# Performance work log

Measured on AMD Instinct MI355X. Metric: run time of the kernel, lower is better.

Reference implementation:

```python
import jax, jax.numpy as jnp
import numpy as np

B, T, C = 4, 2048, 768
H, N = 12, 64
N_LAYER, LAYER_ID = 12, 1
EPS_GN = 0.00064


def setup_inputs():
    key = jax.random.key(0)
    ks = jax.random.split(key, 20)
    r01 = LAYER_ID / (N_LAYER - 1)
    r10 = 1.0 - LAYER_ID / N_LAYER
    ddd = (np.arange(C, dtype=np.float64) / C)[None, None, :]

    def lam(p, off=0.0):
        return jnp.asarray(1.0 - np.power(ddd, p) - off, dtype=jnp.float32)

    decay = -7.0 + 5.0 * (np.arange(C, dtype=np.float64) / (C - 1)) ** (0.85 + r01 ** 0.5)

    def rn(i, shape, scale):
        return scale * jax.random.normal(ks[i], shape, jnp.float32)

    s = 1.0 / C ** 0.5
    return {
        "x": jax.random.normal(ks[0], (B, T, C), jnp.float32),
        "v_first": jax.random.normal(ks[1], (B, T, C), jnp.float32),
        "lambda_r": lam(0.2 * r10), "lambda_w": lam(0.9 * r10),
        "lambda_k": lam(0.9 * r10, 0.4 * r01), "lambda_v": lam(0.4 * r10, 0.6 * r01),
        "lambda_a": lam(0.9 * r10), "lambda_g": lam(0.2 * r10),
        "w_miu": jnp.asarray(decay[None, None, :] + 0.5, jnp.float32),
        "w_A": rn(2, (C, 64), 0.02), "w_B": rn(3, (64, C), 0.02),
        "a_miu": jnp.zeros((1, 1, C), jnp.float32),
        "a_A": rn(4, (C, 64), 0.02), "a_B": rn(5, (64, C), 0.02),
        "v_miu": jnp.ones((1, 1, C), jnp.float32),
        "v_A": rn(6, (C, 64), 0.02), "v_B": rn(7, (64, C), 0.02),
        "g_A": rn(8, (C, 128), 0.02), "g_B": rn(9, (128, C), 0.02),
        "k_k": 0.85 * jnp.ones((1, 1, C), jnp.float32),
        "k_a": jnp.ones((1, 1, C), jnp.float32),
        "r_k": rn(10, (H, N), 0.02),
        "W_r": jax.random.uniform(ks[11], (C, C), jnp.float32, -0.5 * s, 0.5 * s),
        "W_k": jax.random.uniform(ks[12], (C, C), jnp.float32, -0.05 * s, 0.05 * s),
        "W_v": jax.random.uniform(ks[13], (C, C), jnp.float32, -0.5 * s, 0.5 * s),
        "W_o": rn(14, (C, C), 0.02),
        "ln_w": jnp.ones((C,), jnp.float32), "ln_b": jnp.zeros((C,), jnp.float32),
    }


def _wkv7(r, w, k, v, z, b):
    # r,w,k,v,z,b: (B,T,H,N). RWKV-7 linear recurrence with per-head NxN state:
    # S_t = S_{t-1}*diag(exp(-exp(w_t))) + (S_{t-1} z_t) b_t^T + v_t k_t^T ; y_t = S_t r_t
    decay = jnp.exp(-jnp.exp(w))

    def step(S, inp):
        rt, dt, kt, vt, zt, bt = inp  # each (B,H,N)
        sa = jnp.einsum('bhij,bhj->bhi', S, zt)
        S = S * dt[:, :, None, :] + sa[..., None] * bt[:, :, None, :] + vt[..., None] * kt[:, :, None, :]
        y = jnp.einsum('bhij,bhj->bhi', S, rt)
        return S, y

    seq = tuple(jnp.moveaxis(t, 1, 0) for t in (r, decay, k, v, z, b))  # (T,B,H,N)
    S0 = jnp.zeros((r.shape[0], r.shape[2], r.shape[3], r.shape[3]), r.dtype)
    _, ys = jax.lax.scan(step, S0, seq)
    return jnp.moveaxis(ys, 0, 1)  # (B,T,H,N)


def reference(x, v_first, lambda_r, lambda_w, lambda_k, lambda_v, lambda_a, lambda_g,
              w_miu, w_A, w_B, a_miu, a_A, a_B, v_miu, v_A, v_B, g_A, g_B,
              k_k, k_a, r_k, W_r, W_k, W_v, W_o, ln_w, ln_b):
    Bb, Tt, Cc = x.shape
    # ZeroPad2d((0,0,1,-1)): shift sequence right by 1, zero at t=0
    x_shift = jnp.pad(x, ((0, 0), (1, 0), (0, 0)))[:, :-1]
    xd = x_shift - x
    r = (x + xd * lambda_r) @ W_r.T
    w = x + xd * lambda_w
    k = (x + xd * lambda_k) @ W_k.T
    v = (x + xd * lambda_v) @ W_v.T
    a_in = x + xd * lambda_a
    g_in = x + xd * lambda_g
    if LAYER_ID == 0:
        v_first = v
    else:
        v = v + (v_first - v) * jax.nn.sigmoid(v_miu + (v @ v_A) @ v_B)
    w = -jax.nn.softplus(-(w_miu + jnp.tanh(w @ w_A) @ w_B)) - 0.5
    a = jax.nn.sigmoid(a_miu + (a_in @ a_A) @ a_B)
    g = jax.nn.sigmoid(g_in @ g_A) @ g_B
    kk = (k * k_k).reshape(Bb, Tt, H, N)
    kk = kk / jnp.maximum(jnp.linalg.norm(kk, axis=-1, keepdims=True), 1e-12)
    k = k * (1 + (a - 1) * k_a)
    rh = r.reshape(Bb, Tt, H, N)
    wh = w.reshape(Bb, Tt, H, N)
    kh = k.reshape(Bb, Tt, H, N)
    vh = v.reshape(Bb, Tt, H, N)
    ah = a.reshape(Bb, Tt, H, N)
    y = _wkv7(rh, wh, kh, vh, -kk, kk * ah)  # (B,T,H,N)
    # GroupNorm over heads, eps=0.00064, biased variance (torch semantics)
    mu = y.mean(-1, keepdims=True)
    var = y.var(-1, keepdims=True)
    y = ((y - mu) / jnp.sqrt(var + EPS_GN)).reshape(Bb, Tt, Cc) * ln_w + ln_b
    y = y + ((rh * kh * r_k).sum(-1, keepdims=True) * vh).reshape(Bb, Tt, Cc)
    out = (y * g) @ W_o.T
    return (out, v_first)
```

## Files before the change

kernel.cpp:

```cpp
#include <hip/hip_runtime.h>
#include <hip/hip_bf16.h>
#include <math.h>


#define B_  4
#define T_  2048
#define C_  768
#define H_  12

typedef __attribute__((ext_vector_type(8))) short bf16x8;
typedef __attribute__((ext_vector_type(4))) float f32x4;

#define GLD16(gsrc, ldst)                                                     \
  __builtin_amdgcn_global_load_lds(                                           \
      (const __attribute__((address_space(1))) void*)(gsrc),                  \
      (__attribute__((address_space(3))) void*)(ldst), 16, 0, 0)

template <int CTRL>
static __device__ __forceinline__ float row_ror_add(float v) {
  int t = __builtin_amdgcn_update_dpp(0, __float_as_int(v), CTRL, 0xF, 0xF, true);
  return v + __int_as_float(t);
}
static __device__ __forceinline__ float row_sum16(float v) {
  v = row_ror_add<0x128>(v);
  v = row_ror_add<0x124>(v);
  v = row_ror_add<0x122>(v);
  v = row_ror_add<0x121>(v);
  return v;
}

static __device__ __forceinline__ float wave_sum64(float v) {
  v = row_sum16(v);
  v += __shfl_xor(v, 16);
  v += __shfl_xor(v, 32);
  return v;
}

static __device__ __forceinline__ short bf16b(float f) {
  __hip_bfloat16 h = __float2bfloat16(f);
  return *reinterpret_cast<short*>(&h);
}

enum { EPI_NONE = 0, EPI_TANH, EPI_WDECAY, EPI_SIGBIAS, EPI_SIGMOID, EPI_VMIX };

static __device__ __forceinline__ float apply_epi_f(int EPI, float val, int n,
                                                    int gmrow, int N,
                                                    const float* bias,
                                                    const float* ex1,
                                                    const float* ex2) {
  if (EPI == EPI_TANH) {
    val = tanhf(val);
  } else if (EPI == EPI_WDECAY) {
    const float u = bias[n] + val;
    const float sig = 1.f / (1.f + expf(-u));
    val = expf(-0.60653065971263342f * sig);
  } else if (EPI == EPI_SIGBIAS) {
    const float u = bias[n] + val;
    val = 1.f / (1.f + expf(-u));
  } else if (EPI == EPI_SIGMOID) {
    val = 1.f / (1.f + expf(-val));
  } else if (EPI == EPI_VMIX) {
    const float u = bias[n] + val;
    const float sg = 1.f / (1.f + expf(-u));
    const size_t off = (size_t)gmrow * N + n;
    const float v0v = ex1[off];
    const float vf = ex2[off];
    val = v0v + (vf - v0v) * sg;
  }
  return val;
}

template <int EPI, bool DUAL>
__global__ __launch_bounds__(256) void gemm_epi_k(
    const short* __restrict__ A, const short* __restrict__ Bw,
    float* __restrict__ C, short* __restrict__ C16, int M, int N, int K,
    const float* __restrict__ bias, const float* __restrict__ ex1,
    const float* __restrict__ ex2) {
  __shared__ short As[128 * 32];
  __shared__ short Bs[128 * 32];
  const int tid = threadIdx.x;
  const int wave = tid >> 6, lane = tid & 63;
  const int m0 = blockIdx.y * 128, n0 = blockIdx.x * 128;
  const int wm = (wave >> 1) * 64, wn = (wave & 1) * 64;
  const int fr = lane & 15, fk = (lane >> 4) * 8;

  f32x4 acc[4][4];
#pragma unroll
  for (int i = 0; i < 4; i++)
#pragma unroll
    for (int j = 0; j < 4; j++) acc[i][j] = (f32x4){0.f, 0.f, 0.f, 0.f};

  const int srow = tid >> 2, scol = (tid & 3) * 8;
  const short* gA = A + (size_t)(m0 + srow) * K + scol;
  const short* gB = Bw + (size_t)(n0 + srow) * K + scol;
  short* lA0 = &As[wave * 512];
  short* lA1 = &As[2048 + wave * 512];
  short* lB0 = &Bs[wave * 512];
  short* lB1 = &Bs[2048 + wave * 512];

  for (int k0 = 0; k0 < K; k0 += 32) {
    GLD16(gA + k0, lA0);
    GLD16(gA + (size_t)64 * K + k0, lA1);
    GLD16(gB + k0, lB0);
    GLD16(gB + (size_t)64 * K + k0, lB1);
    __syncthreads();

    bf16x8 af[4], bf[4];
#pragma unroll
    for (int i = 0; i < 4; i++)
      af[i] = *(const bf16x8*)&As[(wm + i * 16 + fr) * 32 + fk];
#pragma unroll
    for (int j = 0; j < 4; j++)
      bf[j] = *(const bf16x8*)&Bs[(wn + j * 16 + fr) * 32 + fk];
#pragma unroll
    for (int i = 0; i < 4; i++)
#pragma unroll
      for (int j = 0; j < 4; j++)
        acc[i][j] =
            __builtin_amdgcn_mfma_f32_16x16x32_bf16(af[i], bf[j], acc[i][j], 0, 0, 0);
    __syncthreads();
  }

#pragma unroll
  for (int i = 0; i < 4; i++) {
    const int gm = m0 + wm + i * 16 + (lane >> 4) * 4;
#pragma unroll
    for (int j = 0; j < 4; j++) {
      const int gn = n0 + wn + j * 16 + fr;
#pragma unroll
      for (int rix = 0; rix < 4; rix++) {
        float val = acc[i][j][rix];
        val = apply_epi_f(EPI, val, gn, gm + rix, N, bias, ex1, ex2);
        C[(size_t)(gm + rix) * N + gn] = val;
        if (DUAL) C16[(size_t)(gm + rix) * N + gn] = bf16b(val);
      }
    }
  }
}

template <int EPI>
__global__ __launch_bounds__(256) void gemm_s1_k(
    const short* __restrict__ A, const short* __restrict__ Bw,
    short* __restrict__ out16, int M, int N, int K) {
  __shared__ short As[128 * 32];
  __shared__ short Bs[64 * 32];
  const int tid = threadIdx.x;
  const int wave = tid >> 6, lane = tid & 63;
  const int m0 = blockIdx.y * 128, n0 = blockIdx.x * 64;
  const int wm = (wave >> 1) * 64, wn = (wave & 1) * 32;
  const int fr = lane & 15, fk = (lane >> 4) * 8;

  f32x4 acc[4][2];
#pragma unroll
  for (int i = 0; i < 4; i++)
#pragma unroll
    for (int j = 0; j < 2; j++) acc[i][j] = (f32x4){0.f, 0.f, 0.f, 0.f};

  const int srow = tid >> 2, scol = (tid & 3) * 8;
  const short* gA = A + (size_t)(m0 + srow) * K + scol;
  const short* gB = Bw + (size_t)(n0 + srow) * K + scol;
  short* lA0 = &As[wave * 512];
  short* lA1 = &As[2048 + wave * 512];
  short* lB0 = &Bs[wave * 512];

  for (int k0 = 0; k0 < K; k0 += 32) {
    GLD16(gA + k0, lA0);
    GLD16(gA + (size_t)64 * K + k0, lA1);
    GLD16(gB + k0, lB0);
    __syncthreads();

    bf16x8 af[4], bf[2];
#pragma unroll
    for (int i = 0; i < 4; i++)
      af[i] = *(const bf16x8*)&As[(wm + i * 16 + fr) * 32 + fk];
#pragma unroll
    for (int j = 0; j < 2; j++)
      bf[j] = *(const bf16x8*)&Bs[(wn + j * 16 + fr) * 32 + fk];
#pragma unroll
    for (int i = 0; i < 4; i++)
#pragma unroll
      for (int j = 0; j < 2; j++)
        acc[i][j] =
            __builtin_amdgcn_mfma_f32_16x16x32_bf16(af[i], bf[j], acc[i][j], 0, 0, 0);
    __syncthreads();
  }

#pragma unroll
  for (int i = 0; i < 4; i++) {
    const int gm = m0 + wm + i * 16 + (lane >> 4) * 4;
#pragma unroll
    for (int j = 0; j < 2; j++) {
      const int gn = n0 + wn + j * 16 + fr;
#pragma unroll
      for (int rix = 0; rix < 4; rix++) {
        float val = acc[i][j][rix];
        if (EPI == EPI_TANH) val = tanhf(val);
        else if (EPI == EPI_SIGMOID) val = 1.f / (1.f + expf(-val));
        out16[(size_t)(gm + rix) * N + gn] = bf16b(val);
      }
    }
  }
}

__global__ __launch_bounds__(256) void mix6_k(
    const float* __restrict__ x, const float* __restrict__ lr,
    const float* __restrict__ lk, const float* __restrict__ lv,
    const float* __restrict__ lw, const float* __restrict__ la,
    const float* __restrict__ lg, short* __restrict__ xr,
    short* __restrict__ xk, short* __restrict__ xv, short* __restrict__ xw,
    short* __restrict__ xa, short* __restrict__ xg) {
  const int i = blockIdx.x * 256 + threadIdx.x;
  const int c4 = i % (C_ / 4);
  const int gm = i / (C_ / 4);
  const float4 xa4 = ((const float4*)x)[i];
  float4 xp = make_float4(0.f, 0.f, 0.f, 0.f);
  if ((gm % T_) != 0) xp = ((const float4*)x)[i - C_ / 4];
  const float4 dx =
      make_float4(xp.x - xa4.x, xp.y - xa4.y, xp.z - xa4.z, xp.w - xa4.w);

#define MIXOUT(dst, lam)                                                      \
  {                                                                           \
    const float4 l4 = ((const float4*)lam)[c4];                               \
    short4 o = {bf16b(fmaf(dx.x, l4.x, xa4.x)),                               \
                bf16b(fmaf(dx.y, l4.y, xa4.y)),                               \
                bf16b(fmaf(dx.z, l4.z, xa4.z)),                               \
                bf16b(fmaf(dx.w, l4.w, xa4.w))};                              \
    ((short4*)dst)[i] = o;                                                    \
  }
  MIXOUT(xr, lr);
  MIXOUT(xk, lk);
  MIXOUT(xv, lv);
  MIXOUT(xw, lw);
  MIXOUT(xa, la);
  MIXOUT(xg, lg);
#undef MIXOUT
}

__global__ __launch_bounds__(256) void cvtw4_k(
    const float* __restrict__ w0, const float* __restrict__ w1,
    const float* __restrict__ w2, const float* __restrict__ w3,
    short* __restrict__ o0, short* __restrict__ o1s,
    short* __restrict__ o2s, short* __restrict__ o3s, int n4) {
  const int i = blockIdx.x * 256 + threadIdx.x;
  if (i >= n4) return;
  const float* src;
  short* dst;
  switch (blockIdx.y) {
    case 0: src = w0; dst = o0; break;
    case 1: src = w1; dst = o1s; break;
    case 2: src = w2; dst = o2s; break;
    default: src = w3; dst = o3s; break;
  }
  const float4 v = ((const float4*)src)[i];
  short4 o = {bf16b(v.x), bf16b(v.y), bf16b(v.z), bf16b(v.w)};
  ((short4*)dst)[i] = o;
}

__global__ __launch_bounds__(256) void cvtT8_k(
    const float* __restrict__ i0, const float* __restrict__ i1,
    const float* __restrict__ i2, const float* __restrict__ i3,
    const float* __restrict__ i4, const float* __restrict__ i5,
    const float* __restrict__ i6, const float* __restrict__ i7,
    short* __restrict__ o0, short* __restrict__ o1,
    short* __restrict__ o2, short* __restrict__ o3,
    short* __restrict__ o4, short* __restrict__ o5,
    short* __restrict__ o6, short* __restrict__ o7) {
  const float* in;
  short* out;
  int R, Cc;
  switch (blockIdx.y) {
    case 0: in = i0; out = o0; R = C_; Cc = 64; break;
    case 1: in = i1; out = o1; R = C_; Cc = 64; break;
    case 2: in = i2; out = o2; R = C_; Cc = 64; break;
    case 3: in = i3; out = o3; R = C_; Cc = 128; break;
    case 4: in = i4; out = o4; R = 64; Cc = C_; break;
    case 5: in = i5; out = o5; R = 64; Cc = C_; break;
    case 6: in = i6; out = o6; R = 64; Cc = C_; break;
    default: in = i7; out = o7; R = 128; Cc = C_; break;
  }
  const int n = R * Cc;
  for (int i = blockIdx.x * 256 + threadIdx.x; i < n; i += gridDim.x * 256) {
    const int r = i / Cc, c = i % Cc;
    out[(size_t)c * R + r] = bf16b(in[i]);
  }
}

__global__ __launch_bounds__(256) void kkprep_k(
    const float* __restrict__ k0, const float* __restrict__ a,
    const float* __restrict__ k_k, const float* __restrict__ k_a,
    float* __restrict__ kout, float* __restrict__ z, float* __restrict__ bb) {
  const int wid = threadIdx.x >> 6;
  const int lane = threadIdx.x & 63;
  const size_t hid = (size_t)blockIdx.x * 4 + wid;
  const int h = (int)(hid % H_);
  const size_t idx = hid * 64 + lane;
  const int c = h * 64 + lane;
  const float kv = k0[idx];
  const float av = a[idx];
  const float kk = kv * k_k[c];
  const float ss = wave_sum64(kk * kk);
  const float denom = fmaxf(sqrtf(ss), 1e-12f);
  const float kkn = kk / denom;
  z[idx] = -kkn;
  bb[idx] = kkn * av;
  kout[idx] = kv * (1.f + (av - 1.f) * k_a[c]);
}

#define CH 16
#define NC (T_ / CH)
__global__ __launch_bounds__(256) void wkv7_k(
    const float* __restrict__ rr, const float* __restrict__ dd,
    const float* __restrict__ kk, const float* __restrict__ vv,
    const float* __restrict__ zz, const float* __restrict__ bbv,
    float* __restrict__ yy) {
  __shared__ float lds[2][6 * CH * 64];
  const int blk = blockIdx.x;
  const int bh = blk % 48;
  const int rq = blk / 48;
  const int b = bh / H_, h = bh % H_;
  const int tid = threadIdx.x;
  const int wave = tid >> 6;
  const int l = tid & 63;
  const int l16 = l & 15;
  const int row = rq * 16 + wave * 4 + (l >> 4);
  const int cb = l16 * 4;
  const size_t btb = (size_t)b * T_;

  const size_t g0 = (btb + wave * 4 + (l >> 4)) * C_ + h * 64 + cb;
  const int dbase = wave * 256;

#define STAGE(BUF, GOFF)                                                      \
  {                                                                           \
    float* Ld = &lds[BUF][0];                                                 \
    GLD16(dd + (GOFF), Ld + 0 * 1024 + dbase);                                \
    GLD16(zz + (GOFF), Ld + 1 * 1024 + dbase);                                \
    GLD16(bbv + (GOFF), Ld + 2 * 1024 + dbase);                               \
    GLD16(kk + (GOFF), Ld + 3 * 1024 + dbase);                                \
    GLD16(rr + (GOFF), Ld + 4 * 1024 + dbase);                                \
    GLD16(vv + (GOFF), Ld + 5 * 1024 + dbase);                                \
  }

#define LDSTEP(S_, TL_)                                                       \
  {                                                                           \
    Wf[S_] = *(const float4*)&Lb[0 * 1024 + (TL_) * 64 + cb];                 \
    Zf[S_] = *(const float4*)&Lb[1 * 1024 + (TL_) * 64 + cb];                 \
    Bf[S_] = *(const float4*)&Lb[2 * 1024 + (TL_) * 64 + cb];                 \
    Kf[S_] = *(const float4*)&Lb[3 * 1024 + (TL_) * 64 + cb];                 \
    Rf[S_] = *(const float4*)&Lb[4 * 1024 + (TL_) * 64 + cb];                 \
    Vf[S_] = Lb[5 * 1024 + (TL_) * 64 + row];                                 \
  }

  STAGE(0, g0);
  __syncthreads();

  float S0 = 0.f, S1 = 0.f, S2 = 0.f, S3 = 0.f;
  size_t gpf = g0 + (size_t)CH * C_;
  const size_t ybase = btb * C_ + h * 64 + row;

  for (int c = 0; c < NC; ++c) {
    if (c + 1 < NC) STAGE((c + 1) & 1, gpf);
    gpf += (size_t)CH * C_;
    const float* Lb = lds[c & 1];

    float4 Wf[3], Zf[3], Bf[3], Kf[3], Rf[3];
    float Vf[3];
    LDSTEP(0, 0);
    LDSTEP(1, 1);
#pragma unroll
    for (int tl = 0; tl < CH; ++tl) {
      const int sl = tl % 3;
      if (tl + 2 < CH) {
        const int s2 = (tl + 2) % 3;
        LDSTEP(s2, tl + 2);
      }
      const float4 w4 = Wf[sl], z4 = Zf[sl], b4 = Bf[sl], k4 = Kf[sl],
                   r4 = Rf[sl];
      const float vi = Vf[sl];

      float sa = fmaf(S1, z4.y, S0 * z4.x) + fmaf(S3, z4.w, S2 * z4.z);
      sa = row_sum16(sa);

      S0 = fmaf(S0, w4.x, fmaf(sa, b4.x, vi * k4.x));
      S1 = fmaf(S1, w4.y, fmaf(sa, b4.y, vi * k4.y));
      S2 = fmaf(S2, w4.z, fmaf(sa, b4.z, vi * k4.z));
      S3 = fmaf(S3, w4.w, fmaf(sa, b4.w, vi * k4.w));

      float yp = fmaf(S1, r4.y, S0 * r4.x) + fmaf(S3, r4.w, S2 * r4.z);
      yp = row_sum16(yp);
      if (l16 == 0) yy[ybase + (size_t)(c * CH + tl) * C_] = yp;
    }
    __syncthreads();
  }
#undef STAGE
#undef LDSTEP
}

__global__ __launch_bounds__(256) void gn_k(
    const float* __restrict__ y, const float* __restrict__ r,
    const float* __restrict__ k, const float* __restrict__ v,
    const float* __restrict__ g, const float* __restrict__ r_k,
    const float* __restrict__ ln_w, const float* __restrict__ ln_b,
    short* __restrict__ ymb) {
  const int wid = threadIdx.x >> 6;
  const int lane = threadIdx.x & 63;
  const size_t hid = (size_t)blockIdx.x * 4 + wid;
  const int h = (int)(hid % H_);
  const size_t idx = hid * 64 + lane;
  const int c = h * 64 + lane;

  const float yv = y[idx];
  const float mu = wave_sum64(yv) * (1.f / 64.f);
  const float sq = wave_sum64(yv * yv) * (1.f / 64.f);
  const float var = sq - mu * mu;
  float yn = (yv - mu) * rsqrtf(var + 0.00064f);
  yn = yn * ln_w[c] + ln_b[c];

  const float s = wave_sum64(r[idx] * k[idx] * r_k[c]);
  yn += s * v[idx];
  ymb[idx] = bf16b(yn * g[idx]);
}

__global__ __launch_bounds__(256) void copy4_k(const float4* __restrict__ src,
                                               float4* __restrict__ dst, int n4) {
  const int i = blockIdx.x * blockDim.x + threadIdx.x;
  if (i < n4) dst[i] = src[i];
}

extern "C" void kernel_launch(void* const* d_in, const int* in_sizes, int n_in,
                              void* d_out, int out_size, void* d_ws,
                              size_t ws_size, hipStream_t stream) {
  const float* x       = (const float*)d_in[0];
  const float* v_first = (const float*)d_in[1];
  const float* lam_r   = (const float*)d_in[2];
  const float* lam_w   = (const float*)d_in[3];
  const float* lam_k   = (const float*)d_in[4];
  const float* lam_v   = (const float*)d_in[5];
  const float* lam_a   = (const float*)d_in[6];
  const float* lam_g   = (const float*)d_in[7];
  const float* w_miu   = (const float*)d_in[8];
  const float* w_A     = (const float*)d_in[9];
  const float* w_B     = (const float*)d_in[10];
  const float* a_miu   = (const float*)d_in[11];
  const float* a_A     = (const float*)d_in[12];
  const float* a_B     = (const float*)d_in[13];
  const float* v_miu   = (const float*)d_in[14];
  const float* v_A     = (const float*)d_in[15];
  const float* v_B     = (const float*)d_in[16];
  const float* g_A     = (const float*)d_in[17];
  const float* g_B     = (const float*)d_in[18];
  const float* k_k     = (const float*)d_in[19];
  const float* k_a     = (const float*)d_in[20];
  const float* r_k     = (const float*)d_in[21];
  const float* W_r     = (const float*)d_in[22];
  const float* W_k     = (const float*)d_in[23];
  const float* W_v     = (const float*)d_in[24];
  const float* W_o     = (const float*)d_in[25];
  const float* ln_w    = (const float*)d_in[26];
  const float* ln_b    = (const float*)d_in[27];

  const int M = B_ * T_;
  const size_t S = (size_t)M * C_;

  float* ws   = (float*)d_ws;
  float* r_   = ws + 0 * S;
  float* kbuf = ws + 1 * S;
  float* vbuf = ws + 2 * S;
  float* dec_ = ws + 3 * S;
  float* a_   = ws + 4 * S;
  float* g_   = ws + 5 * S;
  float* z_   = ws + 6 * S;
  float* bb_  = ws + 7 * S;
  float* h_   = ws + 8 * S;
  short* wb   = (short*)(h_ + (size_t)M * 128);
  float* out  = (float*)d_out;

  const int WN = C_ * C_;
  short* wrb = wb + 0 * (size_t)WN;
  short* wkb = wb + 1 * (size_t)WN;
  short* wvb = wb + 2 * (size_t)WN;
  short* wob = wb + 3 * (size_t)WN;
  short* wAT = wb + 4 * (size_t)WN;
  short* aAT = wAT + (size_t)C_ * 64;
  short* vAT = aAT + (size_t)C_ * 64;
  short* gAT = vAT + (size_t)C_ * 64;
  short* wBT = gAT + (size_t)C_ * 128;
  short* aBT = wBT + (size_t)C_ * 64;
  short* vBT = aBT + (size_t)C_ * 64;
  short* gBT = vBT + (size_t)C_ * 64;

  short* xr  = (short*)dec_;
  short* xk  = (short*)a_;
  short* xv  = (short*)g_;
  short* xw  = (short*)z_;
  short* xa  = (short*)z_ + S;
  short* xg  = (short*)bb_;
  short* vbuf16 = (short*)bb_ + S;
  short* h_w = (short*)h_;
  short* h_a = h_w + (size_t)M * 64;
  short* h_g = h_a + (size_t)M * 64;
  short* h_v = (short*)dec_ + S;
  short* ymb = (short*)z_;

  {
    dim3 blk(256), grid(WN / 4 / 256, 4);
    hipLaunchKernelGGL(cvtw4_k, grid, blk, 0, stream, W_r, W_k, W_v, W_o,
                       wrb, wkb, wvb, wob, WN / 4);
  }
  {
    dim3 blk(256), grid((C_ * 128 + 255) / 256, 8);
    hipLaunchKernelGGL(cvtT8_k, grid, blk, 0, stream, w_A, a_A, v_A, g_A,
                       w_B, a_B, v_B, g_B, wAT, aAT, vAT, gAT, wBT, aBT, vBT,
                       gBT);
  }
  {
    dim3 blk(256), grid((int)(S / 4 / 256));
    hipLaunchKernelGGL(mix6_k, grid, blk, 0, stream, x, lam_r, lam_k, lam_v,
                       lam_w, lam_a, lam_g, xr, xk, xv, xw, xa, xg);
  }
  {
    dim3 blk(256), grid(C_ / 128, M / 128);
    hipLaunchKernelGGL((gemm_epi_k<EPI_NONE, false>), grid, blk, 0, stream,
                       xr, wrb, r_, (short*)nullptr, M, C_, C_, nullptr,
                       nullptr, nullptr);
    hipLaunchKernelGGL((gemm_epi_k<EPI_NONE, false>), grid, blk, 0, stream,
                       xk, wkb, kbuf, (short*)nullptr, M, C_, C_, nullptr,
                       nullptr, nullptr);
    hipLaunchKernelGGL((gemm_epi_k<EPI_NONE, true>), grid, blk, 0, stream,
                       xv, wvb, vbuf, vbuf16, M, C_, C_, nullptr, nullptr,
                       nullptr);
  }
  {
    dim3 blk(256);
    dim3 g64(1, M / 128), g128(2, M / 128);
    hipLaunchKernelGGL((gemm_s1_k<EPI_TANH>), g64, blk, 0, stream, xw, wAT,
                       h_w, M, 64, C_);
    hipLaunchKernelGGL((gemm_s1_k<EPI_NONE>), g64, blk, 0, stream, xa, aAT,
                       h_a, M, 64, C_);
    hipLaunchKernelGGL((gemm_s1_k<EPI_SIGMOID>), g128, blk, 0, stream, xg,
                       gAT, h_g, M, 128, C_);
    hipLaunchKernelGGL((gemm_s1_k<EPI_NONE>), g64, blk, 0, stream, vbuf16,
                       vAT, h_v, M, 64, C_);
  }
  {
    dim3 blk(256), grid(C_ / 128, M / 128);
    hipLaunchKernelGGL((gemm_epi_k<EPI_VMIX, false>), grid, blk, 0, stream,
                       h_v, vBT, vbuf, (short*)nullptr, M, C_, 64, v_miu,
                       vbuf, v_first);
    hipLaunchKernelGGL((gemm_epi_k<EPI_WDECAY, false>), grid, blk, 0, stream,
                       h_w, wBT, dec_, (short*)nullptr, M, C_, 64, w_miu,
                       nullptr, nullptr);
    hipLaunchKernelGGL((gemm_epi_k<EPI_SIGBIAS, false>), grid, blk, 0, stream,
                       h_a, aBT, a_, (short*)nullptr, M, C_, 64, a_miu,
                       nullptr, nullptr);
    hipLaunchKernelGGL((gemm_epi_k<EPI_NONE, false>), grid, blk, 0, stream,
                       h_g, gBT, g_, (short*)nullptr, M, C_, 128, nullptr,
                       nullptr, nullptr);
  }
  {
    dim3 grid((B_ * T_ * H_) / 4), blk(256);
    hipLaunchKernelGGL(kkprep_k, grid, blk, 0, stream, kbuf, a_, k_k, k_a,
                       kbuf, z_, bb_);
  }
  {
    dim3 grid(B_ * H_ * 4), blk(256);
    hipLaunchKernelGGL(wkv7_k, grid, blk, 0, stream, r_, dec_, kbuf, vbuf, z_,
                       bb_, a_);
  }
  {
    dim3 grid((B_ * T_ * H_) / 4), blk(256);
    hipLaunchKernelGGL(gn_k, grid, blk, 0, stream, a_, r_, kbuf, vbuf, g_, r_k,
                       ln_w, ln_b, ymb);
  }
  {
    dim3 blk(256), grid(C_ / 128, M / 128);
    hipLaunchKernelGGL((gemm_epi_k<EPI_NONE, false>), grid, blk, 0, stream,
                       ymb, wob, out, (short*)nullptr, M, C_, C_, nullptr,
                       nullptr, nullptr);
  }
  {
    const int n4 = (int)(S / 4);
    dim3 grid((n4 + 255) / 256), blk(256);
    hipLaunchKernelGGL(copy4_k, grid, blk, 0, stream, (const float4*)v_first,
                       (float4*)(out + S), n4);
  }
}
```

Baseline: 754.3 us.

## Batch GEMM launches into multi-role kernels and overlap g-projection with WKV scan

Replaces the many separate GEMM launches with grouped kernels that pick their matrices by block index: r/k/v in one launch, the four low-rank first stages in one, and three second stages in one. The g second-stage GEMM and the v_first copy now run as extra blocks inside the WKV recurrence launch, using GPUs left idle by the 192 scan blocks. The scan reads v straight from global memory into registers, prefetched one chunk ahead, instead of staging it through LDS, and the weight conversions are merged into a single launch. This cuts launch count and idle time, but epilogue selection is now a runtime branch rather than a template parameter, and the 48 g-GEMM blocks loop serially over 8 tiles each, so they may finish after the scan blocks.

Result: faster. 738.4 us (-2.1%).

```diff
diff --git a/kernel.cpp b/kernel.cpp
--- a/kernel.cpp
+++ b/kernel.cpp
@@ -43,23 +43,23 @@
 
 enum { EPI_NONE = 0, EPI_TANH, EPI_WDECAY, EPI_SIGBIAS, EPI_SIGMOID, EPI_VMIX };
 
-static __device__ __forceinline__ float apply_epi_f(int EPI, float val, int n,
+static __device__ __forceinline__ float apply_epi_f(int epi, float val, int n,
                                                     int gmrow, int N,
                                                     const float* bias,
                                                     const float* ex1,
                                                     const float* ex2) {
-  if (EPI == EPI_TANH) {
+  if (epi == EPI_TANH) {
     val = tanhf(val);
-  } else if (EPI == EPI_WDECAY) {
+  } else if (epi == EPI_WDECAY) {
     const float u = bias[n] + val;
     const float sig = 1.f / (1.f + expf(-u));
     val = expf(-0.60653065971263342f * sig);
-  } else if (EPI == EPI_SIGBIAS) {
+  } else if (epi == EPI_SIGBIAS) {
     const float u = bias[n] + val;
     val = 1.f / (1.f + expf(-u));
-  } else if (EPI == EPI_SIGMOID) {
+  } else if (epi == EPI_SIGMOID) {
     val = 1.f / (1.f + expf(-val));
-  } else if (EPI == EPI_VMIX) {
+  } else if (epi == EPI_VMIX) {
     const float u = bias[n] + val;
     const float sg = 1.f / (1.f + expf(-u));
     const size_t off = (size_t)gmrow * N + n;
@@ -70,17 +70,14 @@
   return val;
 }
 
-template <int EPI, bool DUAL>
-__global__ __launch_bounds__(256) void gemm_epi_k(
+static __device__ __forceinline__ void gemm128_tile(
     const short* __restrict__ A, const short* __restrict__ Bw,
     float* __restrict__ C, short* __restrict__ C16, int M, int N, int K,
-    const float* __restrict__ bias, const float* __restrict__ ex1,
-    const float* __restrict__ ex2) {
-  __shared__ short As[128 * 32];
-  __shared__ short Bs[128 * 32];
+    int bx, int by, int epi, const float* bias, const float* ex1,
+    const float* ex2, short* As, short* Bs) {
   const int tid = threadIdx.x;
   const int wave = tid >> 6, lane = tid & 63;
-  const int m0 = blockIdx.y * 128, n0 = blockIdx.x * 128;
+  const int m0 = by * 128, n0 = bx * 128;
   const int wm = (wave >> 1) * 64, wn = (wave & 1) * 64;
   const int fr = lane & 15, fk = (lane >> 4) * 8;
 
@@ -130,23 +127,21 @@
 #pragma unroll
       for (int rix = 0; rix < 4; rix++) {
         float val = acc[i][j][rix];
-        val = apply_epi_f(EPI, val, gn, gm + rix, N, bias, ex1, ex2);
+        val = apply_epi_f(epi, val, gn, gm + rix, N, bias, ex1, ex2);
         C[(size_t)(gm + rix) * N + gn] = val;
-        if (DUAL) C16[(size_t)(gm + rix) * N + gn] = bf16b(val);
+        if (C16) C16[(size_t)(gm + rix) * N + gn] = bf16b(val);
       }
     }
   }
 }
 
-template <int EPI>
-__global__ __launch_bounds__(256) void gemm_s1_k(
+static __device__ __forceinline__ void gemm64_tile(
     const short* __restrict__ A, const short* __restrict__ Bw,
-    short* __restrict__ out16, int M, int N, int K) {
-  __shared__ short As[128 * 32];
-  __shared__ short Bs[64 * 32];
+    short* __restrict__ out16, int M, int N, int K, int bx, int by, int epi,
+    short* As, short* Bs) {
   const int tid = threadIdx.x;
   const int wave = tid >> 6, lane = tid & 63;
-  const int m0 = blockIdx.y * 128, n0 = blockIdx.x * 64;
+  const int m0 = by * 128, n0 = bx * 64;
   const int wm = (wave >> 1) * 64, wn = (wave & 1) * 32;
   const int fr = lane & 15, fk = (lane >> 4) * 8;
 
@@ -194,12 +189,85 @@
 #pragma unroll
       for (int rix = 0; rix < 4; rix++) {
         float val = acc[i][j][rix];
-        if (EPI == EPI_TANH) val = tanhf(val);
-        else if (EPI == EPI_SIGMOID) val = 1.f / (1.f + expf(-val));
+        if (epi == EPI_TANH) val = tanhf(val);
+        else if (epi == EPI_SIGMOID) val = 1.f / (1.f + expf(-val));
         out16[(size_t)(gm + rix) * N + gn] = bf16b(val);
       }
     }
   }
+}
+
+__global__ __launch_bounds__(256) void big3_k(
+    const short* __restrict__ xr, const short* __restrict__ xk,
+    const short* __restrict__ xv, const short* __restrict__ wrb,
+    const short* __restrict__ wkb, const short* __restrict__ wvb,
+    float* __restrict__ r_, float* __restrict__ kbuf,
+    float* __restrict__ vbuf, short* __restrict__ vbuf16) {
+  __shared__ short smem[2 * 128 * 32];
+  const int role = blockIdx.x / 6, bx = blockIdx.x % 6;
+  const short* A;
+  const short* Bw;
+  float* C;
+  short* C16 = nullptr;
+  if (role == 0) { A = xr; Bw = wrb; C = r_; }
+  else if (role == 1) { A = xk; Bw = wkb; C = kbuf; }
+  else { A = xv; Bw = wvb; C = vbuf; C16 = vbuf16; }
+  gemm128_tile(A, Bw, C, C16, B_ * T_, C_, C_, bx, blockIdx.y, EPI_NONE,
+               nullptr, nullptr, nullptr, smem, smem + 128 * 32);
+}
+
+__global__ __launch_bounds__(256) void s1x4_k(
+    const short* __restrict__ xw, const short* __restrict__ xa,
+    const short* __restrict__ xg, const short* __restrict__ vbuf16,
+    const short* __restrict__ wAT, const short* __restrict__ aAT,
+    const short* __restrict__ gAT, const short* __restrict__ vAT,
+    short* __restrict__ h_w, short* __restrict__ h_a,
+    short* __restrict__ h_g, short* __restrict__ h_v) {
+  __shared__ short smem[128 * 32 + 64 * 32];
+  const int bx = blockIdx.x;
+  const short* A;
+  const short* Bw;
+  short* O;
+  int N, tb, epi;
+  if (bx == 0)      { A = xw;     Bw = wAT; O = h_w; N = 64;  tb = 0; epi = EPI_TANH; }
+  else if (bx == 1) { A = xa;     Bw = aAT; O = h_a; N = 64;  tb = 0; epi = EPI_NONE; }
+  else if (bx == 2) { A = xg;     Bw = gAT; O = h_g; N = 128; tb = 0; epi = EPI_SIGMOID; }
+  else if (bx == 3) { A = xg;     Bw = gAT; O = h_g; N = 128; tb = 1; epi = EPI_SIGMOID; }
+  else              { A = vbuf16; Bw = vAT; O = h_v; N = 64;  tb = 0; epi = EPI_NONE; }
+  gemm64_tile(A, Bw, O, B_ * T_, N, C_, tb, blockIdx.y, epi, smem,
+              smem + 128 * 32);
+}
+
+__global__ __launch_bounds__(256) void s2x3_k(
+    const short* __restrict__ h_v, const short* __restrict__ h_w,
+    const short* __restrict__ h_a, const short* __restrict__ vBT,
+    const short* __restrict__ wBT, const short* __restrict__ aBT,
+    float* __restrict__ vbuf, float* __restrict__ dec_, float* __restrict__ a_,
+    const float* __restrict__ v_miu, const float* __restrict__ w_miu,
+    const float* __restrict__ a_miu, const float* __restrict__ v_first) {
+  __shared__ short smem[2 * 128 * 32];
+  const int role = blockIdx.x / 6, bx = blockIdx.x % 6;
+  const short* A;
+  const short* Bw;
+  float* C;
+  const float* bias;
+  const float* ex1 = nullptr;
+  const float* ex2 = nullptr;
+  int epi;
+  if (role == 0) { A = h_v; Bw = vBT; C = vbuf; bias = v_miu; ex1 = vbuf; ex2 = v_first; epi = EPI_VMIX; }
+  else if (role == 1) { A = h_w; Bw = wBT; C = dec_; bias = w_miu; epi = EPI_WDECAY; }
+  else { A = h_a; Bw = aBT; C = a_; bias = a_miu; epi = EPI_SIGBIAS; }
+  gemm128_tile(A, Bw, C, nullptr, B_ * T_, C_, 64, bx, blockIdx.y, epi, bias,
+               ex1, ex2, smem, smem + 128 * 32);
+}
+
+__global__ __launch_bounds__(256) void outp_k(
+    const short* __restrict__ ymb, const short* __restrict__ wob,
+    float* __restrict__ out) {
+  __shared__ short smem[2 * 128 * 32];
+  gemm128_tile(ymb, wob, out, nullptr, B_ * T_, C_, C_, blockIdx.x,
+               blockIdx.y, EPI_NONE, nullptr, nullptr, nullptr, smem,
+               smem + 128 * 32);
 }
 
 __global__ __launch_bounds__(256) void mix6_k(
@@ -236,52 +304,49 @@
 #undef MIXOUT
 }
 
-__global__ __launch_bounds__(256) void cvtw4_k(
-    const float* __restrict__ w0, const float* __restrict__ w1,
-    const float* __restrict__ w2, const float* __restrict__ w3,
-    short* __restrict__ o0, short* __restrict__ o1s,
-    short* __restrict__ o2s, short* __restrict__ o3s, int n4) {
-  const int i = blockIdx.x * 256 + threadIdx.x;
-  if (i >= n4) return;
-  const float* src;
-  short* dst;
-  switch (blockIdx.y) {
-    case 0: src = w0; dst = o0; break;
-    case 1: src = w1; dst = o1s; break;
-    case 2: src = w2; dst = o2s; break;
-    default: src = w3; dst = o3s; break;
-  }
-  const float4 v = ((const float4*)src)[i];
-  short4 o = {bf16b(v.x), bf16b(v.y), bf16b(v.z), bf16b(v.w)};
-  ((short4*)dst)[i] = o;
-}
-
-__global__ __launch_bounds__(256) void cvtT8_k(
-    const float* __restrict__ i0, const float* __restrict__ i1,
-    const float* __restrict__ i2, const float* __restrict__ i3,
-    const float* __restrict__ i4, const float* __restrict__ i5,
-    const float* __restrict__ i6, const float* __restrict__ i7,
-    short* __restrict__ o0, short* __restrict__ o1,
-    short* __restrict__ o2, short* __restrict__ o3,
-    short* __restrict__ o4, short* __restrict__ o5,
-    short* __restrict__ o6, short* __restrict__ o7) {
-  const float* in;
-  short* out;
-  int R, Cc;
-  switch (blockIdx.y) {
-    case 0: in = i0; out = o0; R = C_; Cc = 64; break;
-    case 1: in = i1; out = o1; R = C_; Cc = 64; break;
-    case 2: in = i2; out = o2; R = C_; Cc = 64; break;
-    case 3: in = i3; out = o3; R = C_; Cc = 128; break;
-    case 4: in = i4; out = o4; R = 64; Cc = C_; break;
-    case 5: in = i5; out = o5; R = 64; Cc = C_; break;
-    case 6: in = i6; out = o6; R = 64; Cc = C_; break;
-    default: in = i7; out = o7; R = 128; Cc = C_; break;
-  }
-  const int n = R * Cc;
-  for (int i = blockIdx.x * 256 + threadIdx.x; i < n; i += gridDim.x * 256) {
-    const int r = i / Cc, c = i % Cc;
-    out[(size_t)c * R + r] = bf16b(in[i]);
+__global__ __launch_bounds__(256) void wprep_k(
+    const float* __restrict__ W_r, const float* __restrict__ W_k,
+    const float* __restrict__ W_v, const float* __restrict__ W_o,
+    const float* __restrict__ w_A, const float* __restrict__ a_A,
+    const float* __restrict__ v_A, const float* __restrict__ g_A,
+    const float* __restrict__ w_B, const float* __restrict__ a_B,
+    const float* __restrict__ v_B, const float* __restrict__ g_B,
+    short* __restrict__ wrb, short* __restrict__ wkb,
+    short* __restrict__ wvb, short* __restrict__ wob,
+    short* __restrict__ wAT, short* __restrict__ aAT,
+    short* __restrict__ vAT, short* __restrict__ gAT,
+    short* __restrict__ wBT, short* __restrict__ aBT,
+    short* __restrict__ vBT, short* __restrict__ gBT) {
+  const int job = blockIdx.y;
+  const int WN = C_ * C_;
+  if (job < 4) {
+    const float* src = (job == 0) ? W_r : (job == 1) ? W_k : (job == 2) ? W_v : W_o;
+    short* dst = (job == 0) ? wrb : (job == 1) ? wkb : (job == 2) ? wvb : wob;
+    const int n4 = WN / 4;
+    for (int i = blockIdx.x * 256 + threadIdx.x; i < n4; i += gridDim.x * 256) {
+      const float4 v = ((const float4*)src)[i];
+      short4 o = {bf16b(v.x), bf16b(v.y), bf16b(v.z), bf16b(v.w)};
+      ((short4*)dst)[i] = o;
+    }
+  } else {
+    const float* in;
+    short* out;
+    int R, Cc;
+    switch (job) {
+      case 4: in = w_A; out = wAT; R = C_; Cc = 64; break;
+      case 5: in = a_A; out = aAT; R = C_; Cc = 64; break;
+      case 6: in = v_A; out = vAT; R = C_; Cc = 64; break;
+      case 7: in = g_A; out = gAT; R = C_; Cc = 128; break;
+      case 8: in = w_B; out = wBT; R = 64; Cc = C_; break;
+      case 9: in = a_B; out = aBT; R = 64; Cc = C_; break;
+      case 10: in = v_B; out = vBT; R = 64; Cc = C_; break;
+      default: in = g_B; out = gBT; R = 128; Cc = C_; break;
+    }
+    const int n = R * Cc;
+    for (int i = blockIdx.x * 256 + threadIdx.x; i < n; i += gridDim.x * 256) {
+      const int r = i / Cc, c = i % Cc;
+      out[(size_t)c * R + r] = bf16b(in[i]);
+    }
   }
 }
 
@@ -308,13 +373,35 @@
 
 #define CH 16
 #define NC (T_ / CH)
-__global__ __launch_bounds__(256) void wkv7_k(
+__global__ __launch_bounds__(256) void wkv7f_k(
     const float* __restrict__ rr, const float* __restrict__ dd,
     const float* __restrict__ kk, const float* __restrict__ vv,
     const float* __restrict__ zz, const float* __restrict__ bbv,
-    float* __restrict__ yy) {
-  __shared__ float lds[2][6 * CH * 64];
+    float* __restrict__ yy, const short* __restrict__ h_g,
+    const short* __restrict__ gBT, float* __restrict__ g_,
+    const float4* __restrict__ cpsrc, float4* __restrict__ cpdst, int n4) {
+  __shared__ __align__(16) char smem[2 * 5 * CH * 64 * 4];
   const int blk = blockIdx.x;
+
+  if (blk >= 240) {
+    const int rb = blk - 240;
+    for (int i = rb * 256 + threadIdx.x; i < n4; i += 16 * 256)
+      cpdst[i] = cpsrc[i];
+    return;
+  }
+  if (blk >= 192) {
+    short* As = (short*)smem;
+    short* Bs = As + 128 * 32;
+    const int rb = blk - 192;
+    for (int it = 0; it < 8; ++it) {
+      const int tile = rb + it * 48;
+      gemm128_tile(h_g, gBT, g_, nullptr, B_ * T_, C_, 128, tile % 6,
+                   tile / 6, EPI_NONE, nullptr, nullptr, nullptr, As, Bs);
+    }
+    return;
+  }
+
+  float* lds = (float*)smem;
   const int bh = blk % 48;
   const int rq = blk / 48;
   const int b = bh / H_, h = bh % H_;
@@ -328,16 +415,16 @@
 
   const size_t g0 = (btb + wave * 4 + (l >> 4)) * C_ + h * 64 + cb;
   const int dbase = wave * 256;
+  const size_t vrow0 = btb * C_ + h * 64 + row;
 
 #define STAGE(BUF, GOFF)                                                      \
   {                                                                           \
-    float* Ld = &lds[BUF][0];                                                 \
+    float* Ld = lds + (BUF) * 5120;                                           \
     GLD16(dd + (GOFF), Ld + 0 * 1024 + dbase);                                \
     GLD16(zz + (GOFF), Ld + 1 * 1024 + dbase);                                \
     GLD16(bbv + (GOFF), Ld + 2 * 1024 + dbase);                               \
     GLD16(kk + (GOFF), Ld + 3 * 1024 + dbase);                                \
     GLD16(rr + (GOFF), Ld + 4 * 1024 + dbase);                                \
-    GLD16(vv + (GOFF), Ld + 5 * 1024 + dbase);                                \
   }
 
 #define LDSTEP(S_, TL_)                                                       \
@@ -347,52 +434,72 @@
     Bf[S_] = *(const float4*)&Lb[2 * 1024 + (TL_) * 64 + cb];                 \
     Kf[S_] = *(const float4*)&Lb[3 * 1024 + (TL_) * 64 + cb];                 \
     Rf[S_] = *(const float4*)&Lb[4 * 1024 + (TL_) * 64 + cb];                 \
-    Vf[S_] = Lb[5 * 1024 + (TL_) * 64 + row];                                 \
-  }
-
+  }
+
+#define PREFV(ARR, CC)                                                        \
+  {                                                                           \
+    const size_t vb = vrow0 + (size_t)(CC) * CH * C_;                         \
+    _Pragma("unroll") for (int j = 0; j < CH; ++j)                            \
+        ARR[j] = vv[vb + (size_t)j * C_];                                     \
+  }
+
+#define CHUNK_BODY(VARR, CIDX)                                                \
+  {                                                                           \
+    float4 Wf[3], Zf[3], Bf[3], Kf[3], Rf[3];                                 \
+    LDSTEP(0, 0);                                                             \
+    LDSTEP(1, 1);                                                             \
+    _Pragma("unroll") for (int tl = 0; tl < CH; ++tl) {                       \
+      const int sl = tl % 3;                                                  \
+      if (tl + 2 < CH) { LDSTEP((tl + 2) % 3, tl + 2); }                      \
+      const float4 w4 = Wf[sl], z4 = Zf[sl], b4 = Bf[sl], k4 = Kf[sl],        \
+                   r4 = Rf[sl];                                               \
+      const float vi = VARR[tl];                                              \
+      float sa = fmaf(S1, z4.y, S0 * z4.x) + fmaf(S3, z4.w, S2 * z4.z);       \
+      sa = row_sum16(sa);                                                     \
+      S0 = fmaf(S0, w4.x, fmaf(sa, b4.x, vi * k4.x));                         \
+      S1 = fmaf(S1, w4.y, fmaf(sa, b4.y, vi * k4.y));                         \
+      S2 = fmaf(S2, w4.z, fmaf(sa, b4.z, vi * k4.z));                         \
+      S3 = fmaf(S3, w4.w, fmaf(sa, b4.w, vi * k4.w));                         \
+      float yp = fmaf(S1, r4.y, S0 * r4.x) + fmaf(S3, r4.w, S2 * r4.z);       \
+      yp = row_sum16(yp);                                                     \
+      if (l16 == 0) yy[ybase + (size_t)((CIDX)*CH + tl) * C_] = yp;           \
+    }                                                                         \
+  }
+
+  float vA[CH], vB[CH];
   STAGE(0, g0);
+  PREFV(vA, 0);
   __syncthreads();
 
   float S0 = 0.f, S1 = 0.f, S2 = 0.f, S3 = 0.f;
   size_t gpf = g0 + (size_t)CH * C_;
   const size_t ybase = btb * C_ + h * 64 + row;
 
-  for (int c = 0; c < NC; ++c) {
-    if (c + 1 < NC) STAGE((c + 1) & 1, gpf);
+  for (int c = 0; c < NC; c += 2) {
+    PREFV(vB, c + 1);
+    STAGE(1, gpf);
     gpf += (size_t)CH * C_;
-    const float* Lb = lds[c & 1];
-
-    float4 Wf[3], Zf[3], Bf[3], Kf[3], Rf[3];
-    float Vf[3];
-    LDSTEP(0, 0);
-    LDSTEP(1, 1);
-#pragma unroll
-    for (int tl = 0; tl < CH; ++tl) {
-      const int sl = tl % 3;
-      if (tl + 2 < CH) {
-        const int s2 = (tl + 2) % 3;
-        LDSTEP(s2, tl + 2);
-      }
-      const float4 w4 = Wf[sl], z4 = Zf[sl], b4 = Bf[sl], k4 = Kf[sl],
-                   r4 = Rf[sl];
-      const float vi = Vf[sl];
-
-      float sa = fmaf(S1, z4.y, S0 * z4.x) + fmaf(S3, z4.w, S2 * z4.z);
-      sa = row_sum16(sa);
-
-      S0 = fmaf(S0, w4.x, fmaf(sa, b4.x, vi * k4.x));
-      S1 = fmaf(S1, w4.y, fmaf(sa, b4.y, vi * k4.y));
-      S2 = fmaf(S2, w4.z, fmaf(sa, b4.z, vi * k4.z));
-      S3 = fmaf(S3, w4.w, fmaf(sa, b4.w, vi * k4.w));
-
-      float yp = fmaf(S1, r4.y, S0 * r4.x) + fmaf(S3, r4.w, S2 * r4.z);
-      yp = row_sum16(yp);
-      if (l16 == 0) yy[ybase + (size_t)(c * CH + tl) * C_] = yp;
+    {
+      const float* Lb = lds;
+      CHUNK_BODY(vA, c)
+    }
+    __syncthreads();
+    {
+      const int cn = (c + 2 < NC) ? (c + 2) : (NC - 1);
+      PREFV(vA, cn);
+    }
+    if (c + 2 < NC) STAGE(0, gpf);
+    gpf += (size_t)CH * C_;
+    {
+      const float* Lb = lds + 5120;
+      CHUNK_BODY(vB, c + 1)
     }
     __syncthreads();
   }
 #undef STAGE
 #undef LDSTEP
+#undef PREFV
+#undef CHUNK_BODY
 }
 
 __global__ __launch_bounds__(256) void gn_k(
@@ -418,12 +525,6 @@
   const float s = wave_sum64(r[idx] * k[idx] * r_k[c]);
   yn += s * v[idx];
   ymb[idx] = bf16b(yn * g[idx]);
-}
-
-__global__ __launch_bounds__(256) void copy4_k(const float4* __restrict__ src,
-                                               float4* __restrict__ dst, int n4) {
-  const int i = blockIdx.x * blockDim.x + threadIdx.x;
-  if (i < n4) dst[i] = src[i];
 }
 
 extern "C" void kernel_launch(void* const* d_in, const int* in_sizes, int n_in,
@@ -498,19 +599,14 @@
   short* h_w = (short*)h_;
   short* h_a = h_w + (size_t)M * 64;
   short* h_g = h_a + (size_t)M * 64;
-  short* h_v = (short*)dec_ + S;
+  short* h_v = (short*)g_;
   short* ymb = (short*)z_;
 
   {
-    dim3 blk(256), grid(WN / 4 / 256, 4);
-    hipLaunchKernelGGL(cvtw4_k, grid, blk, 0, stream, W_r, W_k, W_v, W_o,
-                       wrb, wkb, wvb, wob, WN / 4);
-  }
-  {
-    dim3 blk(256), grid((C_ * 128 + 255) / 256, 8);
-    hipLaunchKernelGGL(cvtT8_k, grid, blk, 0, stream, w_A, a_A, v_A, g_A,
-                       w_B, a_B, v_B, g_B, wAT, aAT, vAT, gAT, wBT, aBT, vBT,
-                       gBT);
+    dim3 blk(256), grid(576, 12);
+    hipLaunchKernelGGL(wprep_k, grid, blk, 0, stream, W_r, W_k, W_v, W_o,
+                       w_A, a_A, v_A, g_A, w_B, a_B, v_B, g_B, wrb, wkb, wvb,
+                       wob, wAT, aAT, vAT, gAT, wBT, aBT, vBT, gBT);
   }
   {
     dim3 blk(256), grid((int)(S / 4 / 256));
@@ -518,43 +614,19 @@
                        lam_w, lam_a, lam_g, xr, xk, xv, xw, xa, xg);
   }
   {
-    dim3 blk(256), grid(C_ / 128, M / 128);
-    hipLaunchKernelGGL((gemm_epi_k<EPI_NONE, false>), grid, blk, 0, stream,
-                       xr, wrb, r_, (short*)nullptr, M, C_, C_, nullptr,
-                       nullptr, nullptr);
-    hipLaunchKernelGGL((gemm_epi_k<EPI_NONE, false>), grid, blk, 0, stream,
-                       xk, wkb, kbuf, (short*)nullptr, M, C_, C_, nullptr,
-                       nullptr, nullptr);
-    hipLaunchKernelGGL((gemm_epi_k<EPI_NONE, true>), grid, blk, 0, stream,
-                       xv, wvb, vbuf, vbuf16, M, C_, C_, nullptr, nullptr,
-                       nullptr);
-  }
-  {
-    dim3 blk(256);
-    dim3 g64(1, M / 128), g128(2, M / 128);
-    hipLaunchKernelGGL((gemm_s1_k<EPI_TANH>), g64, blk, 0, stream, xw, wAT,
-                       h_w, M, 64, C_);
-    hipLaunchKernelGGL((gemm_s1_k<EPI_NONE>), g64, blk, 0, stream, xa, aAT,
-                       h_a, M, 64, C_);
-    hipLaunchKernelGGL((gemm_s1_k<EPI_SIGMOID>), g128, blk, 0, stream, xg,
-                       gAT, h_g, M, 128, C_);
-    hipLaunchKernelGGL((gemm_s1_k<EPI_NONE>), g64, blk, 0, stream, vbuf16,
-                       vAT, h_v, M, 64, C_);
-  }
-  {
-    dim3 blk(256), grid(C_ / 128, M / 128);
-    hipLaunchKernelGGL((gemm_epi_k<EPI_VMIX, false>), grid, blk, 0, stream,
-                       h_v, vBT, vbuf, (short*)nullptr, M, C_, 64, v_miu,
-                       vbuf, v_first);
-    hipLaunchKernelGGL((gemm_epi_k<EPI_WDECAY, false>), grid, blk, 0, stream,
-                       h_w, wBT, dec_, (short*)nullptr, M, C_, 64, w_miu,
-                       nullptr, nullptr);
-    hipLaunchKernelGGL((gemm_epi_k<EPI_SIGBIAS, false>), grid, blk, 0, stream,
-                       h_a, aBT, a_, (short*)nullptr, M, C_, 64, a_miu,
-                       nullptr, nullptr);
-    hipLaunchKernelGGL((gemm_epi_k<EPI_NONE, false>), grid, blk, 0, stream,
-                       h_g, gBT, g_, (short*)nullptr, M, C_, 128, nullptr,
-                       nullptr, nullptr);
+    dim3 blk(256), grid(18, M / 128);
+    hipLaunchKernelGGL(big3_k, grid, blk, 0, stream, xr, xk, xv, wrb, wkb,
+                       wvb, r_, kbuf, vbuf, vbuf16);
+  }
+  {
+    dim3 blk(256), grid(5, M / 128);
+    hipLaunchKernelGGL(s1x4_k, grid, blk, 0, stream, xw, xa, xg, vbuf16, wAT,
+                       aAT, gAT, vAT, h_w, h_a, h_g, h_v);
+  }
+  {
+    dim3 blk(256), grid(18, M / 128);
+    hipLaunchKernelGGL(s2x3_k, grid, blk, 0, stream, h_v, h_w, h_a, vBT, wBT,
+                       aBT, vbuf, dec_, a_, v_miu, w_miu, a_miu, v_first);
   }
   {
     dim3 grid((B_ * T_ * H_) / 4), blk(256);
@@ -562,9 +634,10 @@
                        kbuf, z_, bb_);
   }
   {
-    dim3 grid(B_ * H_ * 4), blk(256);
-    hipLaunchKernelGGL(wkv7_k, grid, blk, 0, stream, r_, dec_, kbuf, vbuf, z_,
-                       bb_, a_);
+    dim3 grid(256), blk(256);
+    hipLaunchKernelGGL(wkv7f_k, grid, blk, 0, stream, r_, dec_, kbuf, vbuf,
+                       z_, bb_, a_, h_g, gBT, g_, (const float4*)v_first,
+                       (float4*)(out + S), (int)(S / 4));
   }
   {
     dim3 grid((B_ * T_ * H_) / 4), blk(256);
@@ -573,14 +646,6 @@
   }
   {
     dim3 blk(256), grid(C_ / 128, M / 128);
-    hipLaunchKernelGGL((gemm_epi_k<EPI_NONE, false>), grid, blk, 0, stream,
-                       ymb, wob, out, (short*)nullptr, M, C_, C_, nullptr,
-                       nullptr, nullptr);
-  }
-  {
-    const int n4 = (int)(S / 4);
-    dim3 grid((n4 + 255) / 256), blk(256);
-    hipLaunchKernelGGL(copy4_k, grid, blk, 0, stream, (const float4*)v_first,
-                       (float4*)(out + S), n4);
-  }
-}
+    hipLaunchKernelGGL(outp_k, grid, blk, 0, stream, ymb, wob, out);
+  }
+}
```
